# Kernel tuning notes

Measured on AMD Instinct MI355X. Metric: run time of the kernel, lower is better.

Reference implementation:

```python
import jax, jax.numpy as jnp
import numpy as np

N_LAYER = 2


def setup_inputs() -> dict:
    key = jax.random.key(0)
    k1, k2, k3, k4, k5 = jax.random.split(key, 5)
    N, E, D, C = 50000, 800000, 128, 40
    features = jax.random.normal(k1, (N, D), dtype=jnp.float32)
    adj_row = jax.random.randint(k2, (E,), 0, N, dtype=jnp.int32)
    adj_col = jax.random.randint(k3, (E,), 0, N, dtype=jnp.int32)
    adj_values = jax.random.uniform(k4, (E,), dtype=jnp.float32)
    lin = jax.random.normal(k5, (D, C), dtype=jnp.float32) * (1.0 / np.sqrt(D))
    return {"features": features, "adj_row": adj_row, "adj_col": adj_col,
            "adj_values": adj_values, "lin": lin}


def reference(features, adj_row, adj_col, adj_values, lin):
    N = features.shape[0]
    loop = jnp.arange(N, dtype=adj_row.dtype)
    # preprocess_adj: add self-loops, symmetric GCN normalization D^-1/2 (A+I) D^-1/2
    row = jnp.concatenate([adj_row, loop])
    col = jnp.concatenate([adj_col, loop])
    val = jnp.concatenate([adj_values, jnp.ones((N,), features.dtype)])
    deg = jax.ops.segment_sum(val, row, num_segments=N)
    dinv = jnp.where(deg > 0, jax.lax.rsqrt(jnp.maximum(deg, 1e-12)), 0.0)
    nval = dinv[row] * val * dinv[col]  # normalized edge weights [E+N]
    X = features
    layerwise = []
    for _ in range(N_LAYER):  # X = A_hat @ X (SpMM via gather + segment_sum)
        X = jax.ops.segment_sum(nval[:, None] * X[col], row, num_segments=N)
        layerwise.append(X)
    logits = X @ lin  # [N, out_dim]
    return (jax.nn.log_softmax(logits, axis=1), logits, tuple(layerwise))
```

## Files before the change

### kernel.cpp

```cpp
#include <hip/hip_runtime.h>
#include <math.h>

#define D_FEAT 128
#define SCAN_B 256
#define C_MAX  40
#define FIXP   33554432.0f


__device__ __forceinline__ unsigned bf16_rne(float x) {
    unsigned u = __float_as_uint(x);
    return (u + 0x7fffu + ((u >> 16) & 1u)) >> 16;
}
__device__ __forceinline__ unsigned pack2(float x, float y) {
    return bf16_rne(x) | (bf16_rne(y) << 16);
}
__device__ __forceinline__ float lo_f(unsigned g) { return __uint_as_float(g << 16); }
__device__ __forceinline__ float hi_f(unsigned g) { return __uint_as_float(g & 0xffff0000u); }


__global__ void k_init(unsigned long long* __restrict__ deg64, int N) {
    int i = blockIdx.x * blockDim.x + threadIdx.x;
    if (i < N) deg64[i] = (unsigned long long)(1.0f * FIXP);
}

__global__ void k_deg_hist(const int* __restrict__ row, const float* __restrict__ val,
                           unsigned long long* __restrict__ deg64,
                           int* __restrict__ rank, int E) {
    int e = blockIdx.x * blockDim.x + threadIdx.x;
    if (e >= E) return;
    int r = row[e];
    unsigned long long add = (1ull << 40) |
                             (unsigned long long)(val[e] * FIXP + 0.5f);
    unsigned long long old = atomicAdd(&deg64[r], add);
    rank[e] = (int)(old >> 40);
}


__global__ __launch_bounds__(SCAN_B) void k_part_sum(const unsigned long long* __restrict__ deg64,
                                                     int* __restrict__ part,
                                                     float* __restrict__ dinv,
                                                     int* __restrict__ cnt32, int N) {
    __shared__ int s[SCAN_B];
    int i = blockIdx.x * SCAN_B + threadIdx.x;
    int c = 0;
    if (i < N) {
        unsigned long long p = deg64[i];
        int cntv = (int)(p >> 40);
        float deg = (float)(p & ((1ull << 40) - 1)) * (1.0f / FIXP);
        dinv[i] = rsqrtf(fmaxf(deg, 1e-12f));
        c = (cntv + 7) & ~7;
        cnt32[i] = c;
    }
    s[threadIdx.x] = c;
    __syncthreads();
    for (int off = SCAN_B / 2; off; off >>= 1) {
        if (threadIdx.x < off) s[threadIdx.x] += s[threadIdx.x + off];
        __syncthreads();
    }
    if (threadIdx.x == 0) part[blockIdx.x] = s[0];
}

__global__ __launch_bounds__(SCAN_B) void k_part_scan(int* __restrict__ part, int nchunks,
                                                      int* __restrict__ rowptr, int N) {
    __shared__ int s[SCAN_B];
    int t = threadIdx.x;
    int v = (t < nchunks) ? part[t] : 0;
    s[t] = v;
    __syncthreads();
    for (int off = 1; off < SCAN_B; off <<= 1) {
        int add = (t >= off) ? s[t - off] : 0;
        __syncthreads();
        s[t] += add;
        __syncthreads();
    }
    if (t < nchunks) part[t] = s[t] - v;
    if (t == nchunks - 1) rowptr[N] = s[t];
}

__global__ __launch_bounds__(SCAN_B) void k_chunk_scan(const int* __restrict__ cnt32,
                                                       const int* __restrict__ part,
                                                       int* __restrict__ rowptr, int N) {
    __shared__ int s[SCAN_B];
    int t = threadIdx.x;
    int i = blockIdx.x * SCAN_B + t;
    int v = (i < N) ? cnt32[i] : 0;
    s[t] = v;
    __syncthreads();
    for (int off = 1; off < SCAN_B; off <<= 1) {
        int add = (t >= off) ? s[t - off] : 0;
        __syncthreads();
        s[t] += add;
        __syncthreads();
    }
    if (i < N) rowptr[i] = part[blockIdx.x] + s[t] - v;
}

__global__ void k_convert(const float* __restrict__ X, const float* __restrict__ dinv,
                          unsigned* __restrict__ Xb, int N) {
    int t = blockIdx.x * blockDim.x + threadIdx.x;
    if (t >= N * (D_FEAT / 8)) return;
    float w = dinv[t >> 4];
    float4 a = ((const float4*)X)[t * 2];
    float4 b = ((const float4*)X)[t * 2 + 1];
    uint4 o;
    o.x = pack2(w * a.x, w * a.y); o.y = pack2(w * a.z, w * a.w);
    o.z = pack2(w * b.x, w * b.y); o.w = pack2(w * b.z, w * b.w);
    ((uint4*)Xb)[t] = o;
}

__global__ void k_scatter(const int* __restrict__ row, const int* __restrict__ col,
                          const float* __restrict__ val, const int* __restrict__ rank,
                          const int* __restrict__ rowptr, int2* __restrict__ csr, int E) {
    int e = blockIdx.x * blockDim.x + threadIdx.x;
    if (e >= E) return;
    int r = row[e];
    int pos = rowptr[r] + rank[e];
    csr[pos] = make_int2(col[e], __float_as_int(val[e]));
}


__device__ __forceinline__ float2 spmm_row_bf16(const int* __restrict__ rowptr,
                                                const int2* __restrict__ csr,
                                                const unsigned* __restrict__ Xb,
                                                int rowi, int lane) {
    unsigned gs = Xb[((unsigned)rowi << 6) | lane];
    float2 a0 = make_float2(lo_f(gs), hi_f(gs));
    float2 a1 = make_float2(0.f, 0.f), a2 = make_float2(0.f, 0.f), a3 = make_float2(0.f, 0.f);
    int e  = rowptr[rowi];
    int e1 = rowptr[rowi + 1];
    for (; e < e1; e += 8) {
        const int4* cp = (const int4*)(csr + e);
        int4 q0 = cp[0], q1 = cp[1], q2 = cp[2], q3 = cp[3];
        unsigned g0 = Xb[((unsigned)q0.x << 6) | lane];
        unsigned g1 = Xb[((unsigned)q0.z << 6) | lane];
        unsigned g2 = Xb[((unsigned)q1.x << 6) | lane];
        unsigned g3 = Xb[((unsigned)q1.z << 6) | lane];
        unsigned g4 = Xb[((unsigned)q2.x << 6) | lane];
        unsigned g5 = Xb[((unsigned)q2.z << 6) | lane];
        unsigned g6 = Xb[((unsigned)q3.x << 6) | lane];
        unsigned g7 = Xb[((unsigned)q3.z << 6) | lane];
        float w0_ = __int_as_float(q0.y), w1_ = __int_as_float(q0.w);
        float w2_ = __int_as_float(q1.y), w3_ = __int_as_float(q1.w);
        float w4_ = __int_as_float(q2.y), w5_ = __int_as_float(q2.w);
        float w6_ = __int_as_float(q3.y), w7_ = __int_as_float(q3.w);
        a0.x += w0_ * lo_f(g0); a0.y += w0_ * hi_f(g0);
        a1.x += w1_ * lo_f(g1); a1.y += w1_ * hi_f(g1);
        a2.x += w2_ * lo_f(g2); a2.y += w2_ * hi_f(g2);
        a3.x += w3_ * lo_f(g3); a3.y += w3_ * hi_f(g3);
        a0.x += w4_ * lo_f(g4); a0.y += w4_ * hi_f(g4);
        a1.x += w5_ * lo_f(g5); a1.y += w5_ * hi_f(g5);
        a2.x += w6_ * lo_f(g6); a2.y += w6_ * hi_f(g6);
        a3.x += w7_ * lo_f(g7); a3.y += w7_ * hi_f(g7);
    }
    float2 acc;
    acc.x = (a0.x + a1.x) + (a2.x + a3.x);
    acc.y = (a0.y + a1.y) + (a2.y + a3.y);
    return acc;
}


__global__ __launch_bounds__(256) void k_spmm_l1(const int* __restrict__ rowptr,
                                                 const int2* __restrict__ csr,
                                                 const float* __restrict__ dinv,
                                                 const unsigned* __restrict__ Xb,
                                                 float* __restrict__ Xout,
                                                 unsigned* __restrict__ XbOut, int N) {
    int lane = threadIdx.x & 63;
    int wid  = threadIdx.x >> 6;
    int rowi = blockIdx.x * 4 + wid;
    if (rowi >= N) return;
    float2 acc = spmm_row_bf16(rowptr, csr, Xb, rowi, lane);
    float dr = dinv[rowi];
    float2 x1 = make_float2(dr * acc.x, dr * acc.y);
    ((float2*)Xout)[(size_t)rowi * 64 + lane] = x1;
    XbOut[((unsigned)rowi << 6) | lane] = pack2(dr * x1.x, dr * x1.y);
}

__global__ __launch_bounds__(256) void k_spmm_l2_head(const int* __restrict__ rowptr,
                                                      const int2* __restrict__ csr,
                                                      const float* __restrict__ dinv,
                                                      const unsigned* __restrict__ Xb,
                                                      float* __restrict__ Xout,
                                                      const float* __restrict__ lin,
                                                      float* __restrict__ lsm,
                                                      float* __restrict__ logits,
                                                      int N, int C) {
    __shared__ float lin_s[D_FEAT * C_MAX];
    __shared__ float xs[4][D_FEAT];
    int lane = threadIdx.x & 63;
    int wid  = threadIdx.x >> 6;
    int rowi = blockIdx.x * 4 + wid;

    for (int i = threadIdx.x; i < D_FEAT * C; i += 256) lin_s[i] = lin[i];

    float2 x2 = make_float2(0.f, 0.f);
    if (rowi < N) {
        float2 acc = spmm_row_bf16(rowptr, csr, Xb, rowi, lane);
        float dr = dinv[rowi];
        x2 = make_float2(dr * acc.x, dr * acc.y);
        ((float2*)Xout)[(size_t)rowi * 64 + lane] = x2;
        xs[wid][2 * lane]     = x2.x;
        xs[wid][2 * lane + 1] = x2.y;
    }
    __syncthreads();
    if (rowi >= N) return;

    float a = 0.0f;
    if (lane < C) {
#pragma unroll 8
        for (int d = 0; d < D_FEAT; ++d)
            a += xs[wid][d] * lin_s[d * C + lane];
    }
    float m = (lane < C) ? a : -INFINITY;
    for (int off = 32; off; off >>= 1) m = fmaxf(m, __shfl_xor(m, off));
    float ev = (lane < C) ? __expf(a - m) : 0.0f;
    float s = ev;
    for (int off = 32; off; off >>= 1) s += __shfl_xor(s, off);
    float lse = m + logf(s);
    if (lane < C) {
        logits[(size_t)rowi * C + lane] = a;
        lsm[(size_t)rowi * C + lane]    = a - lse;
    }
}


__global__ __launch_bounds__(256) void k_spmm_f32(const int* __restrict__ rowptr,
                                                  const int2* __restrict__ csr,
                                                  const float* __restrict__ dinv,
                                                  const float* __restrict__ Xin,
                                                  float* __restrict__ Xout, int N) {
    int lane = threadIdx.x & 63;
    int wid  = threadIdx.x >> 6;
    int rowi = blockIdx.x * 4 + wid;
    if (rowi >= N) return;
    const float2* Xin2 = (const float2*)Xin;
    float dr = dinv[rowi];
    float2 v0 = Xin2[(size_t)rowi * 64 + lane];
    float2 a0 = make_float2(dr * v0.x, dr * v0.y);
    float2 a1 = make_float2(0.f, 0.f);
    int e  = rowptr[rowi];
    int e1 = rowptr[rowi + 1];
    for (; e < e1; e += 2) {
        int2 q0 = csr[e], q1 = csr[e + 1];
        float w0 = __int_as_float(q0.y) * dinv[q0.x];
        float w1 = __int_as_float(q1.y) * dinv[q1.x];
        float2 g0 = Xin2[(size_t)(unsigned)q0.x * 64 + lane];
        float2 g1 = Xin2[(size_t)(unsigned)q1.x * 64 + lane];
        a0.x += w0 * g0.x; a0.y += w0 * g0.y;
        a1.x += w1 * g1.x; a1.y += w1 * g1.y;
    }
    float2 acc = make_float2(dr * (a0.x + a1.x), dr * (a0.y + a1.y));
    ((float2*)Xout)[(size_t)rowi * 64 + lane] = acc;
}

__global__ __launch_bounds__(256) void k_head(const float* __restrict__ X,
                                              const float* __restrict__ lin,
                                              float* __restrict__ lsm,
                                              float* __restrict__ logits,
                                              int N, int C) {
    __shared__ float xs[4][D_FEAT];
    int lane = threadIdx.x & 63;
    int wid  = threadIdx.x >> 6;
    int node = blockIdx.x * 4 + wid;
    if (node < N) {
        xs[wid][lane]      = X[(size_t)node * D_FEAT + lane];
        xs[wid][lane + 64] = X[(size_t)node * D_FEAT + 64 + lane];
    }
    __syncthreads();
    if (node >= N) return;

    float acc = 0.0f;
    if (lane < C) {
        for (int d = 0; d < D_FEAT; ++d)
            acc += xs[wid][d] * lin[d * C + lane];
    }
    float m = (lane < C) ? acc : -INFINITY;
    for (int off = 32; off; off >>= 1) m = fmaxf(m, __shfl_xor(m, off));
    float ev = (lane < C) ? __expf(acc - m) : 0.0f;
    float s = ev;
    for (int off = 32; off; off >>= 1) s += __shfl_xor(s, off);
    float lse = m + logf(s);
    if (lane < C) {
        logits[(size_t)node * C + lane] = acc;
        lsm[(size_t)node * C + lane]    = acc - lse;
    }
}


extern "C" void kernel_launch(void* const* d_in, const int* in_sizes, int n_in,
                              void* d_out, int out_size, void* d_ws, size_t ws_size,
                              hipStream_t stream) {
    const float* features = (const float*)d_in[0];
    const int*   adj_row  = (const int*)d_in[1];
    const int*   adj_col  = (const int*)d_in[2];
    const float* adj_val  = (const float*)d_in[3];
    const float* lin      = (const float*)d_in[4];

    const int N = in_sizes[0] / D_FEAT;
    const int E = in_sizes[1];
    const int C = in_sizes[4] / D_FEAT;
    const int csrTot = E + 8 * N;

    float* out = (float*)d_out;
    const size_t NC = (size_t)N * C;
    const size_t ND = (size_t)N * D_FEAT;
    float* lsm    = out;
    float* logits = out + NC;
    float* X1     = out + 2 * NC;
    float* X2     = out + 2 * NC + ND;

    char* wp = (char*)d_ws;
    auto alloc = [&](size_t bytes) { char* p = wp; wp += (bytes + 15) & ~(size_t)15; return p; };
    unsigned long long* deg64 = (unsigned long long*)alloc((size_t)N * 8);
    float*    dinv   = (float*)alloc((size_t)N * 4);
    int*      cnt32  = (int*)alloc((size_t)N * 4);
    int*      rowptr = (int*)alloc((size_t)(N + 1) * 4);
    int*      part   = (int*)alloc(256 * 4);
    int*      rank   = (int*)alloc((size_t)E * 4);
    int2*     csr    = (int2*)alloc((size_t)csrTot * 8);
    unsigned* Xb0    = (unsigned*)alloc((size_t)N * (D_FEAT / 2) * 4);
    unsigned* Xb1    = (unsigned*)alloc((size_t)N * (D_FEAT / 2) * 4);

    const bool bf16_ok = ((size_t)(wp - (char*)d_ws) <= ws_size) && (C <= C_MAX);

    const int B = 256;
    const int nchunks = (N + SCAN_B - 1) / SCAN_B;

    hipMemsetAsync(csr, 0, (size_t)csrTot * 8, stream);
    k_init<<<(N + B - 1) / B, B, 0, stream>>>(deg64, N);
    k_deg_hist<<<(E + B - 1) / B, B, 0, stream>>>(adj_row, adj_val, deg64, rank, E);
    k_part_sum<<<nchunks, SCAN_B, 0, stream>>>(deg64, part, dinv, cnt32, N);
    k_part_scan<<<1, SCAN_B, 0, stream>>>(part, nchunks, rowptr, N);
    k_chunk_scan<<<nchunks, SCAN_B, 0, stream>>>(cnt32, part, rowptr, N);
    k_scatter<<<(E + B - 1) / B, B, 0, stream>>>(adj_row, adj_col, adj_val, rank,
                                                 rowptr, csr, E);

    int spmmBlocks = (N + 3) / 4;
    if (bf16_ok) {
        k_convert<<<(N * (D_FEAT / 8) + B - 1) / B, B, 0, stream>>>(features, dinv, Xb0, N);
        k_spmm_l1<<<spmmBlocks, 256, 0, stream>>>(rowptr, csr, dinv, Xb0, X1, Xb1, N);
        k_spmm_l2_head<<<spmmBlocks, 256, 0, stream>>>(rowptr, csr, dinv, Xb1, X2,
                                                       lin, lsm, logits, N, C);
    } else {
        k_spmm_f32<<<spmmBlocks, 256, 0, stream>>>(rowptr, csr, dinv, features, X1, N);
        k_spmm_f32<<<spmmBlocks, 256, 0, stream>>>(rowptr, csr, dinv, X1, X2, N);
        k_head<<<(N + 3) / 4, 256, 0, stream>>>(X2, lin, lsm, logits, N, C);
    }
}
```

Measured before the change: 183.5 us.

## Gather 16-byte bf16 row chunks per lane with quarter-wave edge split

The SpMM gather is restructured so each 16-lane quarter-wave handles a different edge and each lane loads 16 bytes (8 bf16 features) instead of 4. Partial sums are reduced across quarters with shuffles. The CSR column is pre-shifted to a byte offset so the address needs only an add. The output is written with a permuted lane mapping, and the head GEMV uses float2-packed lin in shared memory. The goal is fewer, wider gather transactions and less address arithmetic, paid for with extra shuffles. The loop assumes rows are padded to multiples of 8 edges, and the shifted column encoding (col<<8) limits node indices to 24 bits.

```diff
diff --git a/kernel.cpp b/kernel.cpp
--- a/kernel.cpp
+++ b/kernel.cpp
@@ -115,47 +115,67 @@
     if (e >= E) return;
     int r = row[e];
     int pos = rowptr[r] + rank[e];
-    csr[pos] = make_int2(col[e], __float_as_int(val[e]));
-}
-
-
-__device__ __forceinline__ float2 spmm_row_bf16(const int* __restrict__ rowptr,
-                                                const int2* __restrict__ csr,
-                                                const unsigned* __restrict__ Xb,
-                                                int rowi, int lane) {
-    unsigned gs = Xb[((unsigned)rowi << 6) | lane];
-    float2 a0 = make_float2(lo_f(gs), hi_f(gs));
-    float2 a1 = make_float2(0.f, 0.f), a2 = make_float2(0.f, 0.f), a3 = make_float2(0.f, 0.f);
-    int e  = rowptr[rowi];
+    csr[pos] = make_int2(col[e] << 8, __float_as_int(val[e]));
+}
+
+
+__device__ __forceinline__ void spmm_row4(const int* __restrict__ rowptr,
+                                          const int4* __restrict__ csr4,
+                                          const char* __restrict__ XbB,
+                                          int rowi, int lane,
+                                          float2& a0, float2& a1,
+                                          float2& a2, float2& a3) {
+    const int g = lane >> 4;
+    const unsigned laneOff = (unsigned)(lane & 15) << 4;
+    int e0 = rowptr[rowi];
     int e1 = rowptr[rowi + 1];
-    for (; e < e1; e += 8) {
-        const int4* cp = (const int4*)(csr + e);
-        int4 q0 = cp[0], q1 = cp[1], q2 = cp[2], q3 = cp[3];
-        unsigned g0 = Xb[((unsigned)q0.x << 6) | lane];
-        unsigned g1 = Xb[((unsigned)q0.z << 6) | lane];
-        unsigned g2 = Xb[((unsigned)q1.x << 6) | lane];
-        unsigned g3 = Xb[((unsigned)q1.z << 6) | lane];
-        unsigned g4 = Xb[((unsigned)q2.x << 6) | lane];
-        unsigned g5 = Xb[((unsigned)q2.z << 6) | lane];
-        unsigned g6 = Xb[((unsigned)q3.x << 6) | lane];
-        unsigned g7 = Xb[((unsigned)q3.z << 6) | lane];
-        float w0_ = __int_as_float(q0.y), w1_ = __int_as_float(q0.w);
-        float w2_ = __int_as_float(q1.y), w3_ = __int_as_float(q1.w);
-        float w4_ = __int_as_float(q2.y), w5_ = __int_as_float(q2.w);
-        float w6_ = __int_as_float(q3.y), w7_ = __int_as_float(q3.w);
-        a0.x += w0_ * lo_f(g0); a0.y += w0_ * hi_f(g0);
-        a1.x += w1_ * lo_f(g1); a1.y += w1_ * hi_f(g1);
-        a2.x += w2_ * lo_f(g2); a2.y += w2_ * hi_f(g2);
-        a3.x += w3_ * lo_f(g3); a3.y += w3_ * hi_f(g3);
-        a0.x += w4_ * lo_f(g4); a0.y += w4_ * hi_f(g4);
-        a1.x += w5_ * lo_f(g5); a1.y += w5_ * hi_f(g5);
-        a2.x += w6_ * lo_f(g6); a2.y += w6_ * hi_f(g6);
-        a3.x += w7_ * lo_f(g7); a3.y += w7_ * hi_f(g7);
-    }
-    float2 acc;
-    acc.x = (a0.x + a1.x) + (a2.x + a3.x);
-    acc.y = (a0.y + a1.y) + (a2.y + a3.y);
-    return acc;
+
+    a0 = make_float2(0.f, 0.f); a1 = make_float2(0.f, 0.f);
+    a2 = make_float2(0.f, 0.f); a3 = make_float2(0.f, 0.f);
+    if (g == 0) {
+        uint4 s = *(const uint4*)(XbB + (((size_t)rowi) << 8) + laneOff);
+        a0 = make_float2(lo_f(s.x), hi_f(s.x));
+        a1 = make_float2(lo_f(s.y), hi_f(s.y));
+        a2 = make_float2(lo_f(s.z), hi_f(s.z));
+        a3 = make_float2(lo_f(s.w), hi_f(s.w));
+    }
+
+    const int4* cp = csr4 + (e0 >> 1) + g;
+    int iters = (e1 - e0) >> 3;
+    for (int it = 0; it < iters; ++it, cp += 4) {
+        int4 qq = *cp;
+        unsigned b1 = (unsigned)qq.x + laneOff;
+        unsigned b2 = (unsigned)qq.z + laneOff;
+        uint4 g1 = *(const uint4*)(XbB + b1);
+        uint4 g2 = *(const uint4*)(XbB + b2);
+        float w1 = __int_as_float(qq.y), w2 = __int_as_float(qq.w);
+        a0.x += w1 * lo_f(g1.x); a0.y += w1 * hi_f(g1.x);
+        a1.x += w1 * lo_f(g1.y); a1.y += w1 * hi_f(g1.y);
+        a2.x += w1 * lo_f(g1.z); a2.y += w1 * hi_f(g1.z);
+        a3.x += w1 * lo_f(g1.w); a3.y += w1 * hi_f(g1.w);
+        a0.x += w2 * lo_f(g2.x); a0.y += w2 * hi_f(g2.x);
+        a1.x += w2 * lo_f(g2.y); a1.y += w2 * hi_f(g2.y);
+        a2.x += w2 * lo_f(g2.z); a2.y += w2 * hi_f(g2.z);
+        a3.x += w2 * lo_f(g2.w); a3.y += w2 * hi_f(g2.w);
+    }
+
+    a0.x += __shfl_xor(a0.x, 16); a0.y += __shfl_xor(a0.y, 16);
+    a1.x += __shfl_xor(a1.x, 16); a1.y += __shfl_xor(a1.y, 16);
+    a2.x += __shfl_xor(a2.x, 16); a2.y += __shfl_xor(a2.y, 16);
+    a3.x += __shfl_xor(a3.x, 16); a3.y += __shfl_xor(a3.y, 16);
+    a0.x += __shfl_xor(a0.x, 32); a0.y += __shfl_xor(a0.y, 32);
+    a1.x += __shfl_xor(a1.x, 32); a1.y += __shfl_xor(a1.y, 32);
+    a2.x += __shfl_xor(a2.x, 32); a2.y += __shfl_xor(a2.y, 32);
+    a3.x += __shfl_xor(a3.x, 32); a3.y += __shfl_xor(a3.y, 32);
+}
+
+__device__ __forceinline__ void store_row_f32(float* __restrict__ Xout, int rowi, int lane,
+                                              float dr, const float2& a0, const float2& a1,
+                                              const float2& a2, const float2& a3) {
+    int g = lane >> 4, c = lane & 15;
+    float2 w = (g == 0) ? a0 : (g == 1) ? a1 : (g == 2) ? a2 : a3;
+    w.x *= dr; w.y *= dr;
+    ((float2*)Xout)[(size_t)rowi * 64 + (c << 2) + g] = w;
 }
 
 
@@ -169,11 +189,19 @@
     int wid  = threadIdx.x >> 6;
     int rowi = blockIdx.x * 4 + wid;
     if (rowi >= N) return;
-    float2 acc = spmm_row_bf16(rowptr, csr, Xb, rowi, lane);
+    float2 a0, a1, a2, a3;
+    spmm_row4(rowptr, (const int4*)csr, (const char*)Xb, rowi, lane, a0, a1, a2, a3);
     float dr = dinv[rowi];
-    float2 x1 = make_float2(dr * acc.x, dr * acc.y);
-    ((float2*)Xout)[(size_t)rowi * 64 + lane] = x1;
-    XbOut[((unsigned)rowi << 6) | lane] = pack2(dr * x1.x, dr * x1.y);
+    store_row_f32(Xout, rowi, lane, dr, a0, a1, a2, a3);
+    if (lane < 16) {
+        float s2 = dr * dr;
+        uint4 o;
+        o.x = pack2(s2 * a0.x, s2 * a0.y);
+        o.y = pack2(s2 * a1.x, s2 * a1.y);
+        o.z = pack2(s2 * a2.x, s2 * a2.y);
+        o.w = pack2(s2 * a3.x, s2 * a3.y);
+        ((uint4*)XbOut)[(size_t)rowi * 16 + lane] = o;
+    }
 }
 
 __global__ __launch_bounds__(256) void k_spmm_l2_head(const int* __restrict__ rowptr,
@@ -185,31 +213,39 @@
                                                       float* __restrict__ lsm,
                                                       float* __restrict__ logits,
                                                       int N, int C) {
-    __shared__ float lin_s[D_FEAT * C_MAX];
-    __shared__ float xs[4][D_FEAT];
+    __shared__ float2 lin2[(D_FEAT / 2) * C_MAX];
+    __shared__ __align__(16) float xs[4][D_FEAT];
     int lane = threadIdx.x & 63;
     int wid  = threadIdx.x >> 6;
     int rowi = blockIdx.x * 4 + wid;
 
-    for (int i = threadIdx.x; i < D_FEAT * C; i += 256) lin_s[i] = lin[i];
-
-    float2 x2 = make_float2(0.f, 0.f);
+    for (int d2 = wid; d2 < D_FEAT / 2; d2 += 4)
+        for (int c = lane; c < C; c += 64)
+            lin2[d2 * C + c] = make_float2(lin[(2 * d2) * C + c],
+                                           lin[(2 * d2 + 1) * C + c]);
+
     if (rowi < N) {
-        float2 acc = spmm_row_bf16(rowptr, csr, Xb, rowi, lane);
+        float2 a0, a1, a2, a3;
+        spmm_row4(rowptr, (const int4*)csr, (const char*)Xb, rowi, lane, a0, a1, a2, a3);
         float dr = dinv[rowi];
-        x2 = make_float2(dr * acc.x, dr * acc.y);
-        ((float2*)Xout)[(size_t)rowi * 64 + lane] = x2;
-        xs[wid][2 * lane]     = x2.x;
-        xs[wid][2 * lane + 1] = x2.y;
+        store_row_f32(Xout, rowi, lane, dr, a0, a1, a2, a3);
+        if (lane < 16) {
+            float4* xv = (float4*)&xs[wid][0];
+            xv[lane * 2]     = make_float4(dr * a0.x, dr * a0.y, dr * a1.x, dr * a1.y);
+            xv[lane * 2 + 1] = make_float4(dr * a2.x, dr * a2.y, dr * a3.x, dr * a3.y);
+        }
     }
     __syncthreads();
     if (rowi >= N) return;
 
+    int cc = (lane < C) ? lane : 0;
+    const float2* xv2 = (const float2*)&xs[wid][0];
     float a = 0.0f;
-    if (lane < C) {
 #pragma unroll 8
-        for (int d = 0; d < D_FEAT; ++d)
-            a += xs[wid][d] * lin_s[d * C + lane];
+    for (int d2 = 0; d2 < D_FEAT / 2; ++d2) {
+        float2 lv = lin2[d2 * C + cc];
+        float2 xv = xv2[d2];
+        a += xv.x * lv.x + xv.y * lv.y;
     }
     float m = (lane < C) ? a : -INFINITY;
     for (int off = 32; off; off >>= 1) m = fmaxf(m, __shfl_xor(m, off));
@@ -242,10 +278,11 @@
     int e1 = rowptr[rowi + 1];
     for (; e < e1; e += 2) {
         int2 q0 = csr[e], q1 = csr[e + 1];
-        float w0 = __int_as_float(q0.y) * dinv[q0.x];
-        float w1 = __int_as_float(q1.y) * dinv[q1.x];
-        float2 g0 = Xin2[(size_t)(unsigned)q0.x * 64 + lane];
-        float2 g1 = Xin2[(size_t)(unsigned)q1.x * 64 + lane];
+        unsigned c0 = (unsigned)q0.x >> 8, c1 = (unsigned)q1.x >> 8;
+        float w0 = __int_as_float(q0.y) * dinv[c0];
+        float w1 = __int_as_float(q1.y) * dinv[c1];
+        float2 g0 = Xin2[(size_t)c0 * 64 + lane];
+        float2 g1 = Xin2[(size_t)c1 * 64 + lane];
         a0.x += w0 * g0.x; a0.y += w0 * g0.y;
         a1.x += w1 * g1.x; a1.y += w1 * g1.y;
     }
```

Measured after the change: 229.5 us. +25.1%, slower.

## Process two rows per wavefront and pre-scale CSR column indices to byte offsets

Applied to the files above, without the earlier changes.

Each wavefront now handles two adjacent rows of the SpMM, interleaving their 8-edge gather batches so twice as many independent loads are in flight. Column indices are stored pre-shifted by 8 (byte offset of a bf16 row), which removes the shift/or work in the gather address math. The f32 fallback is adjusted to decode the shifted index. The aim is to hide gather latency through more memory-level parallelism, at the cost of more registers, lower occupancy, and load imbalance when the two rows differ in degree. The shift also caps node ids at 2^24.

```diff
diff --git a/kernel.cpp b/kernel.cpp
--- a/kernel.cpp
+++ b/kernel.cpp
@@ -115,47 +115,99 @@
     if (e >= E) return;
     int r = row[e];
     int pos = rowptr[r] + rank[e];
-    csr[pos] = make_int2(col[e], __float_as_int(val[e]));
-}
-
-
-__device__ __forceinline__ float2 spmm_row_bf16(const int* __restrict__ rowptr,
-                                                const int2* __restrict__ csr,
-                                                const unsigned* __restrict__ Xb,
-                                                int rowi, int lane) {
-    unsigned gs = Xb[((unsigned)rowi << 6) | lane];
-    float2 a0 = make_float2(lo_f(gs), hi_f(gs));
-    float2 a1 = make_float2(0.f, 0.f), a2 = make_float2(0.f, 0.f), a3 = make_float2(0.f, 0.f);
-    int e  = rowptr[rowi];
-    int e1 = rowptr[rowi + 1];
-    for (; e < e1; e += 8) {
-        const int4* cp = (const int4*)(csr + e);
-        int4 q0 = cp[0], q1 = cp[1], q2 = cp[2], q3 = cp[3];
-        unsigned g0 = Xb[((unsigned)q0.x << 6) | lane];
-        unsigned g1 = Xb[((unsigned)q0.z << 6) | lane];
-        unsigned g2 = Xb[((unsigned)q1.x << 6) | lane];
-        unsigned g3 = Xb[((unsigned)q1.z << 6) | lane];
-        unsigned g4 = Xb[((unsigned)q2.x << 6) | lane];
-        unsigned g5 = Xb[((unsigned)q2.z << 6) | lane];
-        unsigned g6 = Xb[((unsigned)q3.x << 6) | lane];
-        unsigned g7 = Xb[((unsigned)q3.z << 6) | lane];
-        float w0_ = __int_as_float(q0.y), w1_ = __int_as_float(q0.w);
-        float w2_ = __int_as_float(q1.y), w3_ = __int_as_float(q1.w);
-        float w4_ = __int_as_float(q2.y), w5_ = __int_as_float(q2.w);
-        float w6_ = __int_as_float(q3.y), w7_ = __int_as_float(q3.w);
-        a0.x += w0_ * lo_f(g0); a0.y += w0_ * hi_f(g0);
-        a1.x += w1_ * lo_f(g1); a1.y += w1_ * hi_f(g1);
-        a2.x += w2_ * lo_f(g2); a2.y += w2_ * hi_f(g2);
-        a3.x += w3_ * lo_f(g3); a3.y += w3_ * hi_f(g3);
-        a0.x += w4_ * lo_f(g4); a0.y += w4_ * hi_f(g4);
-        a1.x += w5_ * lo_f(g5); a1.y += w5_ * hi_f(g5);
-        a2.x += w6_ * lo_f(g6); a2.y += w6_ * hi_f(g6);
-        a3.x += w7_ * lo_f(g7); a3.y += w7_ * hi_f(g7);
-    }
-    float2 acc;
-    acc.x = (a0.x + a1.x) + (a2.x + a3.x);
-    acc.y = (a0.y + a1.y) + (a2.y + a3.y);
-    return acc;
+    csr[pos] = make_int2(col[e] << 8, __float_as_int(val[e]));
+}
+
+
+struct E8 {
+    unsigned g0, g1, g2, g3, g4, g5, g6, g7;
+    float w0, w1, w2, w3, w4, w5, w6, w7;
+};
+
+__device__ __forceinline__ E8 e8_load(const int2* __restrict__ csr, int e,
+                                      const char* __restrict__ XbB, unsigned lane4) {
+    E8 r;
+    const int4* cp = (const int4*)(csr + e);
+    int4 q0 = cp[0], q1 = cp[1], q2 = cp[2], q3 = cp[3];
+    r.g0 = *(const unsigned*)(XbB + (unsigned)q0.x + lane4);
+    r.g1 = *(const unsigned*)(XbB + (unsigned)q0.z + lane4);
+    r.g2 = *(const unsigned*)(XbB + (unsigned)q1.x + lane4);
+    r.g3 = *(const unsigned*)(XbB + (unsigned)q1.z + lane4);
+    r.g4 = *(const unsigned*)(XbB + (unsigned)q2.x + lane4);
+    r.g5 = *(const unsigned*)(XbB + (unsigned)q2.z + lane4);
+    r.g6 = *(const unsigned*)(XbB + (unsigned)q3.x + lane4);
+    r.g7 = *(const unsigned*)(XbB + (unsigned)q3.z + lane4);
+    r.w0 = __int_as_float(q0.y); r.w1 = __int_as_float(q0.w);
+    r.w2 = __int_as_float(q1.y); r.w3 = __int_as_float(q1.w);
+    r.w4 = __int_as_float(q2.y); r.w5 = __int_as_float(q2.w);
+    r.w6 = __int_as_float(q3.y); r.w7 = __int_as_float(q3.w);
+    return r;
+}
+
+__device__ __forceinline__ void e8_acc(const E8& r, float2& a0, float2& a1,
+                                       float2& a2, float2& a3) {
+    a0.x += r.w0 * lo_f(r.g0); a0.y += r.w0 * hi_f(r.g0);
+    a1.x += r.w1 * lo_f(r.g1); a1.y += r.w1 * hi_f(r.g1);
+    a2.x += r.w2 * lo_f(r.g2); a2.y += r.w2 * hi_f(r.g2);
+    a3.x += r.w3 * lo_f(r.g3); a3.y += r.w3 * hi_f(r.g3);
+    a0.x += r.w4 * lo_f(r.g4); a0.y += r.w4 * hi_f(r.g4);
+    a1.x += r.w5 * lo_f(r.g5); a1.y += r.w5 * hi_f(r.g5);
+    a2.x += r.w6 * lo_f(r.g6); a2.y += r.w6 * hi_f(r.g6);
+    a3.x += r.w7 * lo_f(r.g7); a3.y += r.w7 * hi_f(r.g7);
+}
+
+__device__ __forceinline__ void spmm_pair_bf16(const int* __restrict__ rowptr,
+                                               const int2* __restrict__ csr,
+                                               const char* __restrict__ XbB,
+                                               int rowA, int rowB, int lane,
+                                               float2& outA, float2& outB) {
+    const unsigned lane4 = (unsigned)lane << 2;
+
+    int2 rpA = *(const int2*)(rowptr + rowA);
+    int eA = rpA.x, eA1 = rpA.y;
+    int eB = rowptr[rowB], eB1 = rowptr[rowB + 1];
+
+    unsigned sA = *(const unsigned*)(XbB + ((unsigned)rowA << 8) + lane4);
+    unsigned sB = *(const unsigned*)(XbB + ((unsigned)rowB << 8) + lane4);
+    float2 aA0 = make_float2(lo_f(sA), hi_f(sA));
+    float2 aA1 = make_float2(0.f, 0.f), aA2 = make_float2(0.f, 0.f), aA3 = make_float2(0.f, 0.f);
+    float2 aB0 = make_float2(lo_f(sB), hi_f(sB));
+    float2 aB1 = make_float2(0.f, 0.f), aB2 = make_float2(0.f, 0.f), aB3 = make_float2(0.f, 0.f);
+
+    while (eA + 8 <= eA1 && eB + 8 <= eB1) {
+        E8 ra = e8_load(csr, eA, XbB, lane4);
+        E8 rb = e8_load(csr, eB, XbB, lane4);
+        e8_acc(ra, aA0, aA1, aA2, aA3);
+        e8_acc(rb, aB0, aB1, aB2, aB3);
+        eA += 8; eB += 8;
+    }
+    while (eA + 16 <= eA1) {
+        E8 r0 = e8_load(csr, eA, XbB, lane4);
+        E8 r1 = e8_load(csr, eA + 8, XbB, lane4);
+        e8_acc(r0, aA0, aA1, aA2, aA3);
+        e8_acc(r1, aA0, aA1, aA2, aA3);
+        eA += 16;
+    }
+    if (eA + 8 <= eA1) {
+        E8 r0 = e8_load(csr, eA, XbB, lane4);
+        e8_acc(r0, aA0, aA1, aA2, aA3);
+    }
+    while (eB + 16 <= eB1) {
+        E8 r0 = e8_load(csr, eB, XbB, lane4);
+        E8 r1 = e8_load(csr, eB + 8, XbB, lane4);
+        e8_acc(r0, aB0, aB1, aB2, aB3);
+        e8_acc(r1, aB0, aB1, aB2, aB3);
+        eB += 16;
+    }
+    if (eB + 8 <= eB1) {
+        E8 r0 = e8_load(csr, eB, XbB, lane4);
+        e8_acc(r0, aB0, aB1, aB2, aB3);
+    }
+
+    outA.x = (aA0.x + aA1.x) + (aA2.x + aA3.x);
+    outA.y = (aA0.y + aA1.y) + (aA2.y + aA3.y);
+    outB.x = (aB0.x + aB1.x) + (aB2.x + aB3.x);
+    outB.y = (aB0.y + aB1.y) + (aB2.y + aB3.y);
 }
 
 
@@ -167,13 +219,20 @@
                                                  unsigned* __restrict__ XbOut, int N) {
     int lane = threadIdx.x & 63;
     int wid  = threadIdx.x >> 6;
-    int rowi = blockIdx.x * 4 + wid;
-    if (rowi >= N) return;
-    float2 acc = spmm_row_bf16(rowptr, csr, Xb, rowi, lane);
-    float dr = dinv[rowi];
-    float2 x1 = make_float2(dr * acc.x, dr * acc.y);
-    ((float2*)Xout)[(size_t)rowi * 64 + lane] = x1;
-    XbOut[((unsigned)rowi << 6) | lane] = pack2(dr * x1.x, dr * x1.y);
+    int rowA = blockIdx.x * 8 + wid * 2;
+    if (rowA >= N) return;
+    int rowB = rowA + 1; if (rowB >= N) rowB = rowA;
+
+    float2 accA, accB;
+    spmm_pair_bf16(rowptr, csr, (const char*)Xb, rowA, rowB, lane, accA, accB);
+
+    float dA = dinv[rowA], dB = dinv[rowB];
+    float2 xA = make_float2(dA * accA.x, dA * accA.y);
+    float2 xB = make_float2(dB * accB.x, dB * accB.y);
+    ((float2*)Xout)[(size_t)rowA * 64 + lane] = xA;
+    ((float2*)Xout)[(size_t)rowB * 64 + lane] = xB;
+    XbOut[((unsigned)rowA << 6) | lane] = pack2(dA * xA.x, dA * xA.y);
+    XbOut[((unsigned)rowB << 6) | lane] = pack2(dB * xB.x, dB * xB.y);
 }
 
 __global__ __launch_bounds__(256) void k_spmm_l2_head(const int* __restrict__ rowptr,
@@ -186,40 +245,50 @@
                                                       float* __restrict__ logits,
                                                       int N, int C) {
     __shared__ float lin_s[D_FEAT * C_MAX];
-    __shared__ float xs[4][D_FEAT];
+    __shared__ float xs[8][D_FEAT];
     int lane = threadIdx.x & 63;
     int wid  = threadIdx.x >> 6;
-    int rowi = blockIdx.x * 4 + wid;
+    int rowA = blockIdx.x * 8 + wid * 2;
 
     for (int i = threadIdx.x; i < D_FEAT * C; i += 256) lin_s[i] = lin[i];
 
-    float2 x2 = make_float2(0.f, 0.f);
-    if (rowi < N) {
-        float2 acc = spmm_row_bf16(rowptr, csr, Xb, rowi, lane);
-        float dr = dinv[rowi];
-        x2 = make_float2(dr * acc.x, dr * acc.y);
-        ((float2*)Xout)[(size_t)rowi * 64 + lane] = x2;
-        xs[wid][2 * lane]     = x2.x;
-        xs[wid][2 * lane + 1] = x2.y;
+    if (rowA < N) {
+        int rowB = rowA + 1; if (rowB >= N) rowB = rowA;
+        float2 accA, accB;
+        spmm_pair_bf16(rowptr, csr, (const char*)Xb, rowA, rowB, lane, accA, accB);
+        float dA = dinv[rowA], dB = dinv[rowB];
+        float2 xA = make_float2(dA * accA.x, dA * accA.y);
+        float2 xB = make_float2(dB * accB.x, dB * accB.y);
+        ((float2*)Xout)[(size_t)rowA * 64 + lane] = xA;
+        ((float2*)Xout)[(size_t)rowB * 64 + lane] = xB;
+        xs[wid * 2][2 * lane]         = xA.x;
+        xs[wid * 2][2 * lane + 1]     = xA.y;
+        xs[wid * 2 + 1][2 * lane]     = xB.x;
+        xs[wid * 2 + 1][2 * lane + 1] = xB.y;
     }
     __syncthreads();
-    if (rowi >= N) return;
-
-    float a = 0.0f;
-    if (lane < C) {
+    if (rowA >= N) return;
+
+    int nr = (rowA + 1 < N) ? 2 : 1;
+    for (int r = 0; r < nr; ++r) {
+        int rowi = rowA + r;
+        const float* xrow = xs[wid * 2 + r];
+        float a = 0.0f;
+        if (lane < C) {
 #pragma unroll 8
-        for (int d = 0; d < D_FEAT; ++d)
-            a += xs[wid][d] * lin_s[d * C + lane];
-    }
-    float m = (lane < C) ? a : -INFINITY;
-    for (int off = 32; off; off >>= 1) m = fmaxf(m, __shfl_xor(m, off));
-    float ev = (lane < C) ? __expf(a - m) : 0.0f;
-    float s = ev;
-    for (int off = 32; off; off >>= 1) s += __shfl_xor(s, off);
-    float lse = m + logf(s);
-    if (lane < C) {
-        logits[(size_t)rowi * C + lane] = a;
-        lsm[(size_t)rowi * C + lane]    = a - lse;
+            for (int d = 0; d < D_FEAT; ++d)
+                a += xrow[d] * lin_s[d * C + lane];
+        }
+        float m = (lane < C) ? a : -INFINITY;
+        for (int off = 32; off; off >>= 1) m = fmaxf(m, __shfl_xor(m, off));
+        float ev = (lane < C) ? __expf(a - m) : 0.0f;
+        float s = ev;
+        for (int off = 32; off; off >>= 1) s += __shfl_xor(s, off);
+        float lse = m + logf(s);
+        if (lane < C) {
+            logits[(size_t)rowi * C + lane] = a;
+            lsm[(size_t)rowi * C + lane]    = a - lse;
+        }
     }
 }
 
@@ -242,10 +311,11 @@
     int e1 = rowptr[rowi + 1];
     for (; e < e1; e += 2) {
         int2 q0 = csr[e], q1 = csr[e + 1];
-        float w0 = __int_as_float(q0.y) * dinv[q0.x];
-        float w1 = __int_as_float(q1.y) * dinv[q1.x];
-        float2 g0 = Xin2[(size_t)(unsigned)q0.x * 64 + lane];
-        float2 g1 = Xin2[(size_t)(unsigned)q1.x * 64 + lane];
+        unsigned c0 = (unsigned)q0.x >> 8, c1 = (unsigned)q1.x >> 8;
+        float w0 = __int_as_float(q0.y) * dinv[c0];
+        float w1 = __int_as_float(q1.y) * dinv[c1];
+        float2 g0 = Xin2[(size_t)c0 * 64 + lane];
+        float2 g1 = Xin2[(size_t)c1 * 64 + lane];
         a0.x += w0 * g0.x; a0.y += w0 * g0.y;
         a1.x += w1 * g1.x; a1.y += w1 * g1.y;
     }
@@ -335,13 +405,14 @@
     k_scatter<<<(E + B - 1) / B, B, 0, stream>>>(adj_row, adj_col, adj_val, rank,
                                                  rowptr, csr, E);
 
-    int spmmBlocks = (N + 3) / 4;
     if (bf16_ok) {
+        int spmmBlocks = (N + 7) / 8;
         k_convert<<<(N * (D_FEAT / 8) + B - 1) / B, B, 0, stream>>>(features, dinv, Xb0, N);
         k_spmm_l1<<<spmmBlocks, 256, 0, stream>>>(rowptr, csr, dinv, Xb0, X1, Xb1, N);
         k_spmm_l2_head<<<spmmBlocks, 256, 0, stream>>>(rowptr, csr, dinv, Xb1, X2,
                                                        lin, lsm, logits, N, C);
     } else {
+        int spmmBlocks = (N + 3) / 4;
         k_spmm_f32<<<spmmBlocks, 256, 0, stream>>>(rowptr, csr, dinv, features, X1, N);
         k_spmm_f32<<<spmmBlocks, 256, 0, stream>>>(rowptr, csr, dinv, X1, X2, N);
         k_head<<<(N + 3) / 4, 256, 0, stream>>>(X2, lin, lsm, logits, N, C);
```

Result: slower. 187.6 us (+2.2%).
